# Optimization experiments

Hardware: AMD Instinct MI355X
Metric: run time of the kernel (lower is better)

## Reference

```python
import jax, jax.numpy as jnp
import numpy as np

N, E, D_IN, H, C = 50000, 800000, 128, 4, 32  # C = out_channels // heads

def setup_inputs() -> dict:
    key = jax.random.key(0)
    k1, k2, k3, k4, k5, k6, k7 = jax.random.split(key, 7)
    x = jax.random.normal(k1, (N, D_IN), dtype=jnp.float32)
    # edges guaranteed self-loop-free (matches remove_self_loops on the torch side)
    src = jax.random.randint(k2, (E,), 0, N)
    off = jax.random.randint(k3, (E,), 1, N)
    dst = (src + off) % N
    edge_index = jnp.stack([src, dst]).astype(jnp.int64)
    W = jax.random.normal(k4, (D_IN, H * C), dtype=jnp.float32) * 0.05
    b_lin = jax.random.normal(k5, (H * C,), dtype=jnp.float32) * 0.05
    att = jax.random.normal(k6, (1, H, 2 * C), dtype=jnp.float32) * 0.1
    bias = jnp.zeros((H * C,), dtype=jnp.float32)
    return {"x": x, "edge_index": edge_index, "W": W, "b_lin": b_lin, "att": att, "bias": bias}

def reference(x, edge_index, W, b_lin, att, bias):
    n = x.shape[0]
    # add self loops (every segment nonempty -> safe segment_max)
    loops = jnp.tile(jnp.arange(n, dtype=edge_index.dtype)[None, :], (2, 1))
    ei = jnp.concatenate([edge_index, loops], axis=1)
    e_i, e_j = ei[0], ei[1]  # e_i: destination (softmax/scatter group), e_j: source
    h = (x @ W + b_lin).reshape(n, H, C)  # [N,H,C]
    x_i = h[e_i]  # [E',H,C]
    x_j = h[e_j]
    # attention logits: split att into its x_i / x_j halves to avoid a concat
    a_i, a_j = att[..., :C], att[..., C:]
    logits = (x_i * a_i).sum(-1) + (x_j * a_j).sum(-1)  # [E',H]
    logits = jax.nn.leaky_relu(logits, negative_slope=0.2)
    # segment softmax over destination nodes
    seg_max = jax.ops.segment_max(logits, e_i, num_segments=n)  # [N,H]
    ex = jnp.exp(logits - seg_max[e_i])
    seg_sum = jax.ops.segment_sum(ex, e_i, num_segments=n)
    alpha = ex / seg_sum[e_i]  # [E',H]
    # weighted scatter-sum aggregation
    out = jax.ops.segment_sum(alpha[:, :, None] * x_j, e_i, num_segments=n)  # [N,H,C]
    out = out.reshape(n, H * C) + bias  # concat=True
    return jax.nn.relu(out)
```

## Files before the change

### kernel.cpp

```cpp
#include <hip/hip_runtime.h>
#include <hip/hip_bf16.h>

#define DIN 128
#define HC  128
#define NH  4

#define CHUNK_LOG 14
#define CNK       (1 << CHUNK_LOG)
#define HIST_BYTES 100352

#define GB 256
#define SB 512

typedef __attribute__((ext_vector_type(8))) short short8;
typedef __attribute__((ext_vector_type(4))) float floatx4;

__device__ inline short f2bf_bits(float f) {
    __hip_bfloat16 t = __float2bfloat16(f);
    return *reinterpret_cast<short*>(&t);
}
__device__ inline float bfbits2f(unsigned short u) {
    union { unsigned int i; float f; } c; c.i = ((unsigned int)u) << 16; return c.f;
}

__global__ __launch_bounds__(1024) void hist(
    const int* __restrict__ src, unsigned short* __restrict__ cnt,
    unsigned short* __restrict__ rank16, int n, int E, int total)
{
    __shared__ unsigned int histo[HIST_BYTES / 4];
    const int c = blockIdx.x;
    const int nInts = (n + 1) >> 1;
    for (int u = threadIdx.x; u < nInts; u += 1024) histo[u] = 0u;
    __syncthreads();

    const int e0 = c << CHUNK_LOG;
    const int e1 = min(e0 + CNK, total);
    for (int base = e0; base < e1; base += 4096) {
        int ii[4], ee[4];
        #pragma unroll
        for (int q = 0; q < 4; ++q) {
            const int e = base + q * 1024 + (int)threadIdx.x;
            ee[q] = e;
            ii[q] = (e < e1) ? ((e < E) ? src[e] : (e - E)) : -1;
        }
        #pragma unroll
        for (int q = 0; q < 4; ++q) {
            if (ii[q] >= 0) {
                const unsigned int sh  = (unsigned)(ii[q] & 1) * 16u;
                const unsigned int old = atomicAdd(&histo[ii[q] >> 1], 1u << sh);
                rank16[ee[q]] = (unsigned short)((old >> sh) & 0xffffu);
            }
        }
    }
    __syncthreads();
    unsigned short* row = cnt + (size_t)c * n;
    for (int u = threadIdx.x; u < n; u += 1024)
        row[u] = (unsigned short)((histo[u >> 1] >> ((u & 1) * 16)) & 0xffffu);
}

__global__ __launch_bounds__(256) void scan1(
    unsigned short* __restrict__ cnt, int* __restrict__ rowptr,
    int* __restrict__ bsum, int n, int nchunks)
{
    __shared__ int sh[256];
    const int t = threadIdx.x;
    const int i = blockIdx.x * 256 + t;
    int run = 0;
    if (i < n) {
        for (int c = 0; c < nchunks; ++c) {
            const size_t idx = (size_t)c * n + i;
            const int v = cnt[idx];
            cnt[idx] = (unsigned short)run;
            run += v;
        }
    }
    sh[t] = run;
    __syncthreads();
    #pragma unroll
    for (int off = 1; off < 256; off <<= 1) {
        const int u = (t >= off) ? sh[t - off] : 0;
        __syncthreads();
        sh[t] += u;
        __syncthreads();
    }
    if (i < n) rowptr[i] = sh[t] - run;
    if (t == 255) bsum[blockIdx.x] = sh[255];
}

__global__ __launch_bounds__(1024) void scan2(
    const int* __restrict__ bsum, int* __restrict__ boff, int nb)
{
    __shared__ int sh[1024];
    const int t = threadIdx.x;
    const int v = (t < nb) ? bsum[t] : 0;
    sh[t] = v;
    __syncthreads();
    #pragma unroll
    for (int off = 1; off < 1024; off <<= 1) {
        const int u = (t >= off) ? sh[t - off] : 0;
        __syncthreads();
        sh[t] += u;
        __syncthreads();
    }
    if (t < nb) boff[t] = sh[t] - v;
}

__global__ __launch_bounds__(256) void gemm_scatter(
    const float* __restrict__ x, const float* __restrict__ W,
    const float* __restrict__ b, const float* __restrict__ att,
    __hip_bfloat16* __restrict__ h, float* __restrict__ ali,
    float* __restrict__ alj,
    const int* __restrict__ src, const int* __restrict__ dst,
    const unsigned short* __restrict__ rank16,
    const unsigned short* __restrict__ cnt,
    const int* __restrict__ rowptr, const int* __restrict__ boff,
    unsigned short* __restrict__ csr,
    int n, int ntiles, int E, int total)
{
    __shared__ __hip_bfloat16 Wt[DIN][136];

    if (blockIdx.x >= GB) {
        for (int e = (blockIdx.x - GB) * 256 + threadIdx.x; e < total;
             e += SB * 256) {
            int i, j;
            if (e < E) { i = src[e]; j = dst[e]; }
            else       { i = e - E;  j = i; }
            const int pos = rowptr[i] + boff[i >> 8]
                          + (int)cnt[(size_t)(e >> CHUNK_LOG) * n + i]
                          + (int)rank16[e];
            csr[pos] = (unsigned short)j;
        }
        return;
    }

    for (int idx = threadIdx.x; idx < DIN * HC; idx += 256) {
        const int k = idx >> 7, c = idx & 127;
        Wt[c][k] = __float2bfloat16(W[idx]);
    }
    __syncthreads();

    const int lane = threadIdx.x & 63;
    const int l15 = lane & 15, lg = lane >> 4;

    short8 bf[8][4];
    #pragma unroll
    for (int ct = 0; ct < 8; ++ct)
        #pragma unroll
        for (int ks = 0; ks < 4; ++ks)
            bf[ct][ks] = *(const short8*)(&Wt[ct * 16 + l15][ks * 32 + lg * 8]);

    float bc[8], ai_l[8], aj_l[8];
    #pragma unroll
    for (int ct = 0; ct < 8; ++ct) {
        bc[ct]   = b[ct * 16 + l15];
        ai_l[ct] = att[(ct >> 1) * 64 + (ct & 1) * 16 + l15];
        aj_l[ct] = att[(ct >> 1) * 64 + 32 + (ct & 1) * 16 + l15];
    }

    const int gw = (blockIdx.x * 256 + threadIdx.x) >> 6;
    const int nw = (GB * 256) >> 6;
    for (int tile = gw; tile < ntiles; tile += nw) {
        int row = tile * 16 + l15;
        if (row >= n) row = n - 1;
        floatx4 acc[8];
        #pragma unroll
        for (int ct = 0; ct < 8; ++ct) acc[ct] = (floatx4)0.f;

        #pragma unroll
        for (int ks = 0; ks < 4; ++ks) {
            const float4 f0 = *(const float4*)(x + (size_t)row * DIN + ks * 32 + lg * 8);
            const float4 f1 = *(const float4*)(x + (size_t)row * DIN + ks * 32 + lg * 8 + 4);
            short8 af;
            af[0] = f2bf_bits(f0.x); af[1] = f2bf_bits(f0.y);
            af[2] = f2bf_bits(f0.z); af[3] = f2bf_bits(f0.w);
            af[4] = f2bf_bits(f1.x); af[5] = f2bf_bits(f1.y);
            af[6] = f2bf_bits(f1.z); af[7] = f2bf_bits(f1.w);
            #pragma unroll
            for (int ct = 0; ct < 8; ++ct)
                acc[ct] = __builtin_amdgcn_mfma_f32_16x16x32_bf16(
                    af, bf[ct][ks], acc[ct], 0, 0, 0);
        }

        #pragma unroll
        for (int reg = 0; reg < 4; ++reg) {
            const int r = tile * 16 + lg * 4 + reg;

            #pragma unroll
            for (int ct = 0; ct < 8; ++ct)
                if (r < n)
                    h[(size_t)r * HC + ct * 16 + l15] =
                        __float2bfloat16(acc[ct][reg] + bc[ct]);

            float pi[4], pj[4];
            #pragma unroll
            for (int hd = 0; hd < 4; ++hd) {
                float vi = 0.f, vj = 0.f;
                #pragma unroll
                for (int q = 0; q < 2; ++q) {
                    const int ct = hd * 2 + q;
                    const float hv = acc[ct][reg] + bc[ct];
                    vi = fmaf(hv, ai_l[ct], vi);
                    vj = fmaf(hv, aj_l[ct], vj);
                }
                #pragma unroll
                for (int m = 1; m <= 8; m <<= 1) {
                    vi += __shfl_xor(vi, m);
                    vj += __shfl_xor(vj, m);
                }
                pi[hd] = vi; pj[hd] = vj;
            }
            if (l15 < 8 && r < n) {
                const int hd = l15 & 3;
                float wi = pi[0];
                wi = (hd == 1) ? pi[1] : wi;
                wi = (hd == 2) ? pi[2] : wi;
                wi = (hd == 3) ? pi[3] : wi;
                float wj = pj[0];
                wj = (hd == 1) ? pj[1] : wj;
                wj = (hd == 2) ? pj[2] : wj;
                wj = (hd == 3) ? pj[3] : wj;
                if (l15 < 4) ali[(size_t)r * 4 + hd] = wi;
                else         alj[(size_t)r * 4 + hd] = wj;
            }
        }
    }
}

__global__ __launch_bounds__(256) void aggregate_csr(
    const int* __restrict__ rowptr, const int* __restrict__ boff,
    const unsigned short* __restrict__ csr,
    const float* __restrict__ ali, const float* __restrict__ alj,
    const __hip_bfloat16* __restrict__ h, const float* __restrict__ bias,
    float* __restrict__ out, int n, int total)
{
    const int lane = threadIdx.x & 63;
    const int l32  = lane & 31;
    const int half = lane >> 5;
    const int hh   = l32 >> 3;
    const int gp = (blockIdx.x * 256 + threadIdx.x) >> 6;
    const int np = (gridDim.x * 256) >> 6;
    const unsigned short* hu = (const unsigned short*)h;
    const float b0 = bias[l32 * 4 + 0], b1 = bias[l32 * 4 + 1];
    const float b2 = bias[l32 * 4 + 2], b3 = bias[l32 * 4 + 3];

    for (int p = gp; p * 2 < n; p += np) {
        const int i = p * 2 + half;
        if (i >= n) continue;
        const int rs = rowptr[i] + boff[i >> 8];
        const int re = (i + 1 == n) ? total
                                    : rowptr[i + 1] + boff[(i + 1) >> 8];
        const float aii = ali[(size_t)i * 4 + hh];

        float a0 = 0.f, a1 = 0.f, a2 = 0.f, a3 = 0.f, s = 0.f;
        int t = rs;
        for (; t + 8 <= re; t += 8) {
            int jj[8]; float ll[8]; ushort4 uu[8];
            #pragma unroll
            for (int q = 0; q < 8; ++q) jj[q] = csr[t + q];
            #pragma unroll
            for (int q = 0; q < 8; ++q) ll[q] = alj[(size_t)jj[q] * 4 + hh];
            #pragma unroll
            for (int q = 0; q < 8; ++q)
                uu[q] = *(const ushort4*)(hu + (size_t)jj[q] * HC + l32 * 4);
            #pragma unroll
            for (int q = 0; q < 8; ++q) {
                float l = aii + ll[q];
                l = l > 0.f ? l : 0.2f * l;
                const float ex = __expf(l);
                s += ex;
                a0 = fmaf(ex, bfbits2f(uu[q].x), a0);
                a1 = fmaf(ex, bfbits2f(uu[q].y), a1);
                a2 = fmaf(ex, bfbits2f(uu[q].z), a2);
                a3 = fmaf(ex, bfbits2f(uu[q].w), a3);
            }
        }
        for (; t + 4 <= re; t += 4) {
            int jj[4]; float ll[4]; ushort4 uu[4];
            #pragma unroll
            for (int q = 0; q < 4; ++q) jj[q] = csr[t + q];
            #pragma unroll
            for (int q = 0; q < 4; ++q) ll[q] = alj[(size_t)jj[q] * 4 + hh];
            #pragma unroll
            for (int q = 0; q < 4; ++q)
                uu[q] = *(const ushort4*)(hu + (size_t)jj[q] * HC + l32 * 4);
            #pragma unroll
            for (int q = 0; q < 4; ++q) {
                float l = aii + ll[q];
                l = l > 0.f ? l : 0.2f * l;
                const float ex = __expf(l);
                s += ex;
                a0 = fmaf(ex, bfbits2f(uu[q].x), a0);
                a1 = fmaf(ex, bfbits2f(uu[q].y), a1);
                a2 = fmaf(ex, bfbits2f(uu[q].z), a2);
                a3 = fmaf(ex, bfbits2f(uu[q].w), a3);
            }
        }
        for (; t < re; ++t) {
            const int j = csr[t];
            float l = aii + alj[(size_t)j * 4 + hh];
            l = l > 0.f ? l : 0.2f * l;
            const float ex = __expf(l);
            s += ex;
            const ushort4 u = *(const ushort4*)(hu + (size_t)j * HC + l32 * 4);
            a0 = fmaf(ex, bfbits2f(u.x), a0);
            a1 = fmaf(ex, bfbits2f(u.y), a1);
            a2 = fmaf(ex, bfbits2f(u.z), a2);
            a3 = fmaf(ex, bfbits2f(u.w), a3);
        }
        const float inv = 1.0f / s;
        float o0 = fmaf(a0, inv, b0);
        float o1 = fmaf(a1, inv, b1);
        float o2 = fmaf(a2, inv, b2);
        float o3 = fmaf(a3, inv, b3);
        float4 ov;
        ov.x = o0 > 0.f ? o0 : 0.f;
        ov.y = o1 > 0.f ? o1 : 0.f;
        ov.z = o2 > 0.f ? o2 : 0.f;
        ov.w = o3 > 0.f ? o3 : 0.f;
        *(float4*)(out + (size_t)i * HC + l32 * 4) = ov;
    }
}

extern "C" void kernel_launch(void* const* d_in, const int* in_sizes, int n_in,
                              void* d_out, int out_size, void* d_ws, size_t ws_size,
                              hipStream_t stream)
{
    const float* x    = (const float*)d_in[0];
    const int*   ei   = (const int*)d_in[1];
    const float* W    = (const float*)d_in[2];
    const float* b    = (const float*)d_in[3];
    const float* att  = (const float*)d_in[4];
    const float* bias = (const float*)d_in[5];

    const int n     = in_sizes[0] / DIN;
    const int E     = in_sizes[1] / 2;
    const int total = E + n;

    const int* src = ei;
    const int* dst = ei + E;

    const int nchunks = (total + CNK - 1) >> CHUNK_LOG;
    const int nb      = (n + 255) / 256;

    char* ws = (char*)d_ws;
    size_t off = 0;
    auto take = [&](size_t bytes) {
        char* p = ws + off;
        off += (bytes + 255) & ~(size_t)255;
        return p;
    };
    __hip_bfloat16* h   = (__hip_bfloat16*)take((size_t)n * HC * 2);
    float* ali    = (float*)take((size_t)n * NH * 4);
    float* alj    = (float*)take((size_t)n * NH * 4);
    int*   rowptr = (int*)take((size_t)(n + 1) * 4);
    int*   bsum   = (int*)take((size_t)nb * 4);
    int*   boff   = (int*)take((size_t)nb * 4);
    unsigned short* cnt    = (unsigned short*)take((size_t)nchunks * n * 2);
    unsigned short* rank16 = (unsigned short*)take((size_t)total * 2);
    unsigned short* csr    = (unsigned short*)take((size_t)total * 2);

    float* out = (float*)d_out;

    hist<<<nchunks, 1024, 0, stream>>>(src, cnt, rank16, n, E, total);
    scan1<<<nb, 256, 0, stream>>>(cnt, rowptr, bsum, n, nchunks);
    scan2<<<1, 1024, 0, stream>>>(bsum, boff, nb);

    const int ntiles = (n + 15) / 16;
    gemm_scatter<<<GB + SB, 256, 0, stream>>>(
        x, W, b, att, h, ali, alj,
        src, dst, rank16, cnt, rowptr, boff, csr,
        n, ntiles, E, total);

    const int pairBlocks = ((n + 1) / 2 + 3) / 4;
    aggregate_csr<<<pairBlocks, 256, 0, stream>>>(rowptr, boff, csr, ali, alj,
                                                  h, bias, out, n, total);
}
```

Before: 97.84 us.

## Split each node's edges across both wave halves and double histogram chunk size

The aggregation kernel now gives each node a full 64-lane wavefront instead of half of one. The two halves handle alternating edges, and their partial sums are combined with a cross-half shuffle before one half writes the output. This should balance per-node edge lists better and expose more memory-level parallelism, at the cost of twice as many waves and a shuffle reduction per node. The histogram chunk size is also doubled, which halves the number of chunks and the size of the count/scan work.

```diff
diff --git a/kernel.cpp b/kernel.cpp
--- a/kernel.cpp
+++ b/kernel.cpp
@@ -5,7 +5,7 @@
 #define HC  128
 #define NH  4
 
-#define CHUNK_LOG 14
+#define CHUNK_LOG 15
 #define CNK       (1 << CHUNK_LOG)
 #define HIST_BYTES 100352
 
@@ -237,47 +237,24 @@
     const int l32  = lane & 31;
     const int half = lane >> 5;
     const int hh   = l32 >> 3;
-    const int gp = (blockIdx.x * 256 + threadIdx.x) >> 6;
-    const int np = (gridDim.x * 256) >> 6;
+    const int gw = (blockIdx.x * 256 + threadIdx.x) >> 6;
+    const int nw = (gridDim.x * 256) >> 6;
     const unsigned short* hu = (const unsigned short*)h;
     const float b0 = bias[l32 * 4 + 0], b1 = bias[l32 * 4 + 1];
     const float b2 = bias[l32 * 4 + 2], b3 = bias[l32 * 4 + 3];
 
-    for (int p = gp; p * 2 < n; p += np) {
-        const int i = p * 2 + half;
-        if (i >= n) continue;
+    for (int i = gw; i < n; i += nw) {
         const int rs = rowptr[i] + boff[i >> 8];
         const int re = (i + 1 == n) ? total
                                     : rowptr[i + 1] + boff[(i + 1) >> 8];
         const float aii = ali[(size_t)i * 4 + hh];
 
         float a0 = 0.f, a1 = 0.f, a2 = 0.f, a3 = 0.f, s = 0.f;
-        int t = rs;
-        for (; t + 8 <= re; t += 8) {
-            int jj[8]; float ll[8]; ushort4 uu[8];
-            #pragma unroll
-            for (int q = 0; q < 8; ++q) jj[q] = csr[t + q];
-            #pragma unroll
-            for (int q = 0; q < 8; ++q) ll[q] = alj[(size_t)jj[q] * 4 + hh];
-            #pragma unroll
-            for (int q = 0; q < 8; ++q)
-                uu[q] = *(const ushort4*)(hu + (size_t)jj[q] * HC + l32 * 4);
-            #pragma unroll
-            for (int q = 0; q < 8; ++q) {
-                float l = aii + ll[q];
-                l = l > 0.f ? l : 0.2f * l;
-                const float ex = __expf(l);
-                s += ex;
-                a0 = fmaf(ex, bfbits2f(uu[q].x), a0);
-                a1 = fmaf(ex, bfbits2f(uu[q].y), a1);
-                a2 = fmaf(ex, bfbits2f(uu[q].z), a2);
-                a3 = fmaf(ex, bfbits2f(uu[q].w), a3);
-            }
-        }
-        for (; t + 4 <= re; t += 4) {
+        int t = rs + half;
+        for (; t + 6 < re; t += 8) {
             int jj[4]; float ll[4]; ushort4 uu[4];
             #pragma unroll
-            for (int q = 0; q < 4; ++q) jj[q] = csr[t + q];
+            for (int q = 0; q < 4; ++q) jj[q] = csr[t + q * 2];
             #pragma unroll
             for (int q = 0; q < 4; ++q) ll[q] = alj[(size_t)jj[q] * 4 + hh];
             #pragma unroll
@@ -295,7 +272,7 @@
                 a3 = fmaf(ex, bfbits2f(uu[q].w), a3);
             }
         }
-        for (; t < re; ++t) {
+        for (; t < re; t += 2) {
             const int j = csr[t];
             float l = aii + alj[(size_t)j * 4 + hh];
             l = l > 0.f ? l : 0.2f * l;
@@ -307,17 +284,26 @@
             a2 = fmaf(ex, bfbits2f(u.z), a2);
             a3 = fmaf(ex, bfbits2f(u.w), a3);
         }
-        const float inv = 1.0f / s;
-        float o0 = fmaf(a0, inv, b0);
-        float o1 = fmaf(a1, inv, b1);
-        float o2 = fmaf(a2, inv, b2);
-        float o3 = fmaf(a3, inv, b3);
-        float4 ov;
-        ov.x = o0 > 0.f ? o0 : 0.f;
-        ov.y = o1 > 0.f ? o1 : 0.f;
-        ov.z = o2 > 0.f ? o2 : 0.f;
-        ov.w = o3 > 0.f ? o3 : 0.f;
-        *(float4*)(out + (size_t)i * HC + l32 * 4) = ov;
+
+        a0 += __shfl_xor(a0, 32);
+        a1 += __shfl_xor(a1, 32);
+        a2 += __shfl_xor(a2, 32);
+        a3 += __shfl_xor(a3, 32);
+        s  += __shfl_xor(s, 32);
+
+        if (half == 0) {
+            const float inv = 1.0f / s;
+            float o0 = fmaf(a0, inv, b0);
+            float o1 = fmaf(a1, inv, b1);
+            float o2 = fmaf(a2, inv, b2);
+            float o3 = fmaf(a3, inv, b3);
+            float4 ov;
+            ov.x = o0 > 0.f ? o0 : 0.f;
+            ov.y = o1 > 0.f ? o1 : 0.f;
+            ov.z = o2 > 0.f ? o2 : 0.f;
+            ov.w = o3 > 0.f ? o3 : 0.f;
+            *(float4*)(out + (size_t)i * HC + l32 * 4) = ov;
+        }
     }
 }
 
@@ -371,7 +357,7 @@
         src, dst, rank16, cnt, rowptr, boff, csr,
         n, ntiles, E, total);
 
-    const int pairBlocks = ((n + 1) / 2 + 3) / 4;
-    aggregate_csr<<<pairBlocks, 256, 0, stream>>>(rowptr, boff, csr, ali, alj,
+    const int nodeBlocks = (n + 3) / 4;
+    aggregate_csr<<<nodeBlocks, 256, 0, stream>>>(rowptr, boff, csr, ali, alj,
                                                   h, bias, out, n, total);
 }
```

Result: faster. 94.20 us, median of 2 (-3.7%).
